# Performance work log

Hardware: AMD Instinct MI355X
Metric: run time of the kernel (lower is better)

Reference implementation:

```python
import jax, jax.numpy as jnp
import numpy as np

ITERN = 5  # hard-coded SqrtmLayer(cov_mat, 5)


def setup_inputs() -> dict:
    key = jax.random.key(0)
    k1, k2, k3 = jax.random.split(key, 3)
    B, C, H, W = 16, 64, 256, 256
    R = 8  # reduction
    x = jax.random.normal(k1, (B, C, H, W), dtype=jnp.float32)
    w1 = jax.random.normal(k2, (C // R, C), dtype=jnp.float32) * 0.1
    b1 = jnp.zeros((C // R,), dtype=jnp.float32)
    w2 = jax.random.normal(k3, (C, C // R), dtype=jnp.float32) * 0.1
    b2 = jnp.zeros((C,), dtype=jnp.float32)
    return {"x": x, "w1": w1, "b1": b1, "w2": w2, "b2": b2}


def _covpool(x):
    # x: [B, C, h, w].  y = x @ I_hat @ x^T with I_hat = (1/M)I - (1/M^2)J,
    # which equals centered covariance: (x_c @ x_c^T) / M.
    B, C, h, w = x.shape
    M = h * w
    xf = x.reshape(B, C, M)
    xc = xf - jnp.mean(xf, axis=-1, keepdims=True)
    return jnp.einsum('bcm,bdm->bcd', xc, xc) / M  # [B, C, C]


def _sqrtm_ns(cov, iterN):
    # Newton-Schulz iteration for matrix square root (per-batch [C,C]).
    B, C, _ = cov.shape
    I = jnp.eye(C, dtype=cov.dtype)
    I3 = 3.0 * I
    normA = jnp.einsum('bii->b', cov)  # trace
    A = cov / normA[:, None, None]
    ZY = 0.5 * (I3 - A)
    Y = jnp.matmul(A, ZY)
    Z = ZY
    for _ in range(1, iterN - 1):
        ZY = 0.5 * (I3 - jnp.matmul(Z, Y))
        Y = jnp.matmul(Y, ZY)
        Z = jnp.matmul(ZY, Z)
    ZY = 0.5 * jnp.matmul(Y, I3 - jnp.matmul(Z, Y))
    return ZY * jnp.sqrt(normA)[:, None, None]


def reference(x, w1, b1, w2, b2):
    # h,w < 1000 so the crop branch is identity (x_sub = x)
    cov = _covpool(x)                       # [B, C, C]
    cov_sqrt = _sqrtm_ns(cov, ITERN)        # [B, C, C]
    v = jnp.mean(cov_sqrt, axis=1)          # [B, C] (mean over rows, dim=1)
    hid = jax.nn.relu(jnp.einsum('bc,hc->bh', v, w1) + b1)
    att = jax.nn.sigmoid(jnp.einsum('bh,ch->bc', hid, w2) + b2)
    return att[:, :, None, None] * x
```

## Files before the change

kernel.cpp:

```cpp
#include <hip/hip_runtime.h>
#include <hip/hip_bf16.h>
#include <math.h>

#define BATCH 16
#define CH    64
#define MM    65536
#define PSTRIDE 4160
#define SF    68

typedef __attribute__((ext_vector_type(8))) short s16x8;
typedef __attribute__((ext_vector_type(4))) float f32x4;

__device__ __forceinline__ unsigned short f2bf(float f) {
    __hip_bfloat16 h = __float2bfloat16(f);
    return __builtin_bit_cast(unsigned short, h);
}
__device__ __forceinline__ float bf2f(unsigned short u) {
    return __builtin_bit_cast(float, (unsigned)u << 16);
}

__global__ __launch_bounds__(256, 3) void gram_mfma(const float* __restrict__ x,
                                                    float* __restrict__ part,
                                                    int nchunk, int chunk_m) {
    int blk = blockIdx.x;
    int b = blk / nchunk, chunk = blk - b * nchunk;
    int t = threadIdx.x, w = t >> 6, l = t & 63;
    int lr = l & 15, lg = l >> 4;
    int mwave = chunk_m >> 2;
    int nck = mwave >> 5;

    const float* xw = x + (size_t)b * CH * MM + (size_t)chunk * chunk_m +
                      (size_t)w * mwave + lg * 8;
    const float* rp0 = xw + (size_t)(lr)      * MM;
    const float* rp1 = xw + (size_t)(16 + lr) * MM;
    const float* rp2 = xw + (size_t)(32 + lr) * MM;
    const float* rp3 = xw + (size_t)(48 + lr) * MM;

    f32x4 acc[10];
    f32x4 accs[4];
    const f32x4 zero = {0.f, 0.f, 0.f, 0.f};
#pragma unroll
    for (int i = 0; i < 10; ++i) acc[i] = zero;
#pragma unroll
    for (int i = 0; i < 4; ++i) accs[i] = zero;

    s16x8 ones;
    {
        unsigned short* op1 = (unsigned short*)&ones;
#pragma unroll
        for (int i = 0; i < 8; ++i) op1[i] = 0x3F80;
    }

    float4 A0, A1, A2, A3, A4, A5, A6, A7;
    float4 B0, B1, B2, B3, B4, B5, B6, B7;

#define LOAD8(P, o) do {                                                      \
        P##0 = *(const float4*)(rp0 + (o));  P##1 = *(const float4*)(rp0 + (o) + 4); \
        P##2 = *(const float4*)(rp1 + (o));  P##3 = *(const float4*)(rp1 + (o) + 4); \
        P##4 = *(const float4*)(rp2 + (o));  P##5 = *(const float4*)(rp2 + (o) + 4); \
        P##6 = *(const float4*)(rp3 + (o));  P##7 = *(const float4*)(rp3 + (o) + 4); \
    } while (0)

#define CVT_ROW(va, vb, fr) do {                                              \
        unsigned short* fp = (unsigned short*)&(fr);                          \
        fp[0] = f2bf((va).x); fp[1] = f2bf((va).y);                           \
        fp[2] = f2bf((va).z); fp[3] = f2bf((va).w);                           \
        fp[4] = f2bf((vb).x); fp[5] = f2bf((vb).y);                           \
        fp[6] = f2bf((vb).z); fp[7] = f2bf((vb).w);                           \
    } while (0)

#define COMPUTE(P) do {                                                       \
        s16x8 fr0, fr1, fr2, fr3;                                             \
        CVT_ROW(P##0, P##1, fr0);                                             \
        CVT_ROW(P##2, P##3, fr1);                                             \
        CVT_ROW(P##4, P##5, fr2);                                             \
        CVT_ROW(P##6, P##7, fr3);                                             \
        acc[0] = __builtin_amdgcn_mfma_f32_16x16x32_bf16(fr0, fr0, acc[0], 0, 0, 0); \
        acc[1] = __builtin_amdgcn_mfma_f32_16x16x32_bf16(fr0, fr1, acc[1], 0, 0, 0); \
        acc[2] = __builtin_amdgcn_mfma_f32_16x16x32_bf16(fr0, fr2, acc[2], 0, 0, 0); \
        acc[3] = __builtin_amdgcn_mfma_f32_16x16x32_bf16(fr0, fr3, acc[3], 0, 0, 0); \
        acc[4] = __builtin_amdgcn_mfma_f32_16x16x32_bf16(fr1, fr1, acc[4], 0, 0, 0); \
        acc[5] = __builtin_amdgcn_mfma_f32_16x16x32_bf16(fr1, fr2, acc[5], 0, 0, 0); \
        acc[6] = __builtin_amdgcn_mfma_f32_16x16x32_bf16(fr1, fr3, acc[6], 0, 0, 0); \
        acc[7] = __builtin_amdgcn_mfma_f32_16x16x32_bf16(fr2, fr2, acc[7], 0, 0, 0); \
        acc[8] = __builtin_amdgcn_mfma_f32_16x16x32_bf16(fr2, fr3, acc[8], 0, 0, 0); \
        acc[9] = __builtin_amdgcn_mfma_f32_16x16x32_bf16(fr3, fr3, acc[9], 0, 0, 0); \
        accs[0] = __builtin_amdgcn_mfma_f32_16x16x32_bf16(ones, fr0, accs[0], 0, 0, 0); \
        accs[1] = __builtin_amdgcn_mfma_f32_16x16x32_bf16(ones, fr1, accs[1], 0, 0, 0); \
        accs[2] = __builtin_amdgcn_mfma_f32_16x16x32_bf16(ones, fr2, accs[2], 0, 0, 0); \
        accs[3] = __builtin_amdgcn_mfma_f32_16x16x32_bf16(ones, fr3, accs[3], 0, 0, 0); \
    } while (0)

    LOAD8(A, 0);
    for (int c = 0; c < nck; c += 2) {
        LOAD8(B, (c + 1) * 32);
        COMPUTE(A);
        if (c + 2 < nck) LOAD8(A, (c + 2) * 32);
        COMPUTE(B);
    }

#define UIDX(i, j) ((i) * 4 + (j) - ((i) * ((i) + 1)) / 2)

    __shared__ float xs[64 * 65];
    __shared__ float csum[64];
    for (int ww = 0; ww < 4; ++ww) {
        if (w == ww) {
#pragma unroll
            for (int i = 0; i < 4; ++i)
#pragma unroll
                for (int j = 0; j < 4; ++j)
                    if (i <= j) {
#pragma unroll
                        for (int jj = 0; jj < 4; ++jj) {
                            int r = i * 16 + lg * 4 + jj, cc = j * 16 + lr;
                            float v = acc[UIDX(i, j)][jj];
                            if (ww == 0) xs[r * 65 + cc] = v;
                            else         xs[r * 65 + cc] += v;
                        }
                    }
            if (l < 16) {
                if (ww == 0) {
                    csum[l]      = accs[0][0]; csum[16 + l] = accs[1][0];
                    csum[32 + l] = accs[2][0]; csum[48 + l] = accs[3][0];
                } else {
                    csum[l]      += accs[0][0]; csum[16 + l] += accs[1][0];
                    csum[32 + l] += accs[2][0]; csum[48 + l] += accs[3][0];
                }
            }
        }
        __syncthreads();
    }

    float* op = part + (size_t)blk * PSTRIDE;
#pragma unroll
    for (int rix = 0; rix < 16; ++rix) {
        int e = t + rix * 256;
        int r = e >> 6, cc = e & 63;
        float v = ((r >> 4) > (cc >> 4)) ? xs[cc * 65 + r] : xs[r * 65 + cc];
        __builtin_nontemporal_store(v, op + e);
    }
    if (t < 64) __builtin_nontemporal_store(csum[t], op + 4096 + t);
}

__global__ __launch_bounds__(256) void reduce_parts(const float* __restrict__ part,
                                                    float* __restrict__ red,
                                                    int nchunk) {
    int b = blockIdx.y;
    int i = blockIdx.x * 256 + threadIdx.x;
    if (i >= PSTRIDE / 4) return;
    const f32x4* p = reinterpret_cast<const f32x4*>(part + (size_t)b * nchunk * PSTRIDE) + i;
    f32x4 s = {0.f, 0.f, 0.f, 0.f};
    for (int ch = 0; ch < nchunk; ++ch) {
        f32x4 v = __builtin_nontemporal_load(p + (size_t)ch * (PSTRIDE / 4));
        s += v;
    }
    reinterpret_cast<f32x4*>(red + (size_t)b * PSTRIDE)[i] = s;
}

__device__ __forceinline__ void cvt_store(const float* __restrict__ M, int row,
                                          int col, unsigned short* Hp,
                                          unsigned short* Lp) {
    float4 v = *reinterpret_cast<const float4*>(M + row * SF + col);
    ushort4 h, lo;
    h.x = f2bf(v.x); lo.x = f2bf(v.x - bf2f(h.x));
    h.y = f2bf(v.y); lo.y = f2bf(v.y - bf2f(h.y));
    h.z = f2bf(v.z); lo.z = f2bf(v.z - bf2f(h.z));
    h.w = f2bf(v.w); lo.w = f2bf(v.w - bf2f(h.w));
    int byte = (row * 128 + col * 2) ^ ((row & 7) << 4);
    *reinterpret_cast<ushort4*>(reinterpret_cast<char*>(Hp) + byte) = h;
    *reinterpret_cast<ushort4*>(reinterpret_cast<char*>(Lp) + byte) = lo;
}

__device__ __forceinline__ void mm64(const float* __restrict__ A,
                                     const float* __restrict__ B,
                                     float* __restrict__ C,
                                     unsigned short* AHp, unsigned short* ALp,
                                     unsigned short* BHp, unsigned short* BLp,
                                     int t) {
    int w = t >> 6, l = t & 63, lg = l >> 4, lr = l & 15;
    __syncthreads();
#pragma unroll
    for (int r = 0; r < 4; ++r) {
        int e4 = t + r * 256;
        int row = e4 >> 4;
        int col = (e4 & 15) << 2;
        cvt_store(A, row, col, AHp, ALp);
        cvt_store(B, row, col, BHp, BLp);
    }
    __syncthreads();
    f32x4 acc[4];
    const f32x4 zero = {0.f, 0.f, 0.f, 0.f};
#pragma unroll
    for (int i = 0; i < 4; ++i) acc[i] = zero;
    int arow = w * 16 + lr;
#pragma unroll
    for (int kk = 0; kk < 2; ++kk) {
        int kbyte = kk * 64 + lg * 16;
        int abyte = (arow * 128 + kbyte) ^ ((arow & 7) << 4);
        s16x8 ah = *reinterpret_cast<const s16x8*>(reinterpret_cast<const char*>(AHp) + abyte);
        s16x8 al = *reinterpret_cast<const s16x8*>(reinterpret_cast<const char*>(ALp) + abyte);
#pragma unroll
        for (int ct = 0; ct < 4; ++ct) {
            int brow = ct * 16 + lr;
            int bbyte = (brow * 128 + kbyte) ^ ((brow & 7) << 4);
            s16x8 bh = *reinterpret_cast<const s16x8*>(reinterpret_cast<const char*>(BHp) + bbyte);
            s16x8 bl = *reinterpret_cast<const s16x8*>(reinterpret_cast<const char*>(BLp) + bbyte);
            acc[ct] = __builtin_amdgcn_mfma_f32_16x16x32_bf16(ah, bh, acc[ct], 0, 0, 0);
            acc[ct] = __builtin_amdgcn_mfma_f32_16x16x32_bf16(ah, bl, acc[ct], 0, 0, 0);
            acc[ct] = __builtin_amdgcn_mfma_f32_16x16x32_bf16(al, bh, acc[ct], 0, 0, 0);
        }
    }
#pragma unroll
    for (int ct = 0; ct < 4; ++ct)
#pragma unroll
        for (int j = 0; j < 4; ++j)
            C[(w * 16 + lg * 4 + j) * SF + ct * 16 + lr] = acc[ct][j];
    __syncthreads();
}

__global__ __launch_bounds__(256) void ns_att(const float* __restrict__ red,
                                              const float* __restrict__ w1,
                                              const float* __restrict__ b1,
                                              const float* __restrict__ w2,
                                              const float* __restrict__ b2,
                                              float* __restrict__ att) {
    __shared__ float BUF[5][64 * SF];
    __shared__ unsigned short AH[64 * 64], AL[64 * 64], BH[64 * 64], BL[64 * 64];
    __shared__ float sv[64];
    __shared__ float hid8[8];
    __shared__ float scal[2];

    int b = blockIdx.x, t = threadIdx.x;
    const float* pb = red + (size_t)b * PSTRIDE;

    if (t < 64) sv[t] = pb[4096 + t];
    __syncthreads();

    const float invM = 1.0f / (float)MM;
    const float invM2 = invM * invM;
#pragma unroll
    for (int r = 0; r < 4; ++r) {
        int e4 = t + r * 256;
        int row = e4 >> 4;
        int col = (e4 & 15) << 2;
        float4 g = *(reinterpret_cast<const float4*>(pb) + e4);
        float sr = sv[row] * invM2;
        BUF[0][row * SF + col]     = g.x * invM - sr * sv[col];
        BUF[0][row * SF + col + 1] = g.y * invM - sr * sv[col + 1];
        BUF[0][row * SF + col + 2] = g.z * invM - sr * sv[col + 2];
        BUF[0][row * SF + col + 3] = g.w * invM - sr * sv[col + 3];
    }
    __syncthreads();

    if (t == 0) {
        float tr = 0.f;
        for (int c = 0; c < 64; ++c) tr += BUF[0][c * SF + c];
        scal[0] = 1.0f / tr;
        scal[1] = sqrtf(tr);
    }
    __syncthreads();
    float itr = scal[0];
#pragma unroll
    for (int rr = 0; rr < 16; ++rr) {
        int e = t + rr * 256;
        BUF[0][(e >> 6) * SF + (e & 63)] *= itr;
    }

    float *pA = BUF[0], *pY = BUF[1], *pZ = BUF[2], *pT = BUF[3], *pS = BUF[4];

    mm64(pA, pA, pT, AH, AL, BH, BL, t);
#pragma unroll
    for (int rr = 0; rr < 16; ++rr) {
        int e = t + rr * 256;
        int r = e >> 6, c = e & 63;
        float a = pA[r * SF + c];
        pY[r * SF + c] = 1.5f * a - 0.5f * pT[r * SF + c];
        pZ[r * SF + c] = (r == c ? 1.5f : 0.f) - 0.5f * a;
    }

    for (int it = 0; it < 3; ++it) {
        mm64(pZ, pY, pT, AH, AL, BH, BL, t);
#pragma unroll
        for (int rr = 0; rr < 16; ++rr) {
            int e = t + rr * 256;
            int r = e >> 6, c = e & 63;
            pT[r * SF + c] = (r == c ? 1.5f : 0.f) - 0.5f * pT[r * SF + c];
        }
        mm64(pY, pT, pS, AH, AL, BH, BL, t);
        mm64(pT, pZ, pA, AH, AL, BH, BL, t);
        float* tmp;
        tmp = pY; pY = pS; pS = tmp;
        tmp = pZ; pZ = pA; pA = tmp;
    }
    mm64(pZ, pY, pT, AH, AL, BH, BL, t);
#pragma unroll
    for (int rr = 0; rr < 16; ++rr) {
        int e = t + rr * 256;
        int r = e >> 6, c = e & 63;
        pT[r * SF + c] = (r == c ? 1.5f : 0.f) - 0.5f * pT[r * SF + c];
    }
    mm64(pY, pT, pS, AH, AL, BH, BL, t);

    if (t < 64) {
        float v = 0.f;
        for (int i = 0; i < 64; ++i) v += pS[t * SF + i];
        sv[t] = v * scal[1] * (1.0f / 64.0f);
    }
    __syncthreads();
    if (t < 8) {
        float h = b1[t];
        for (int c = 0; c < 64; ++c) h += sv[c] * w1[t * 64 + c];
        hid8[t] = h > 0.f ? h : 0.f;
    }
    __syncthreads();
    if (t < 64) {
        float p = b2[t];
        for (int h = 0; h < 8; ++h) p += hid8[h] * w2[t * 8 + h];
        att[b * 64 + t] = 1.0f / (1.0f + expf(-p));
    }
}

__global__ __launch_bounds__(256) void scale_out(const float* __restrict__ x,
                                                 const float* __restrict__ att,
                                                 float* __restrict__ out) {
    size_t i = (size_t)blockIdx.x * blockDim.x + threadIdx.x;
    const size_t total4 = (size_t)BATCH * CH * MM / 4;
    const size_t stride = (size_t)gridDim.x * blockDim.x;
    const f32x4* x4 = reinterpret_cast<const f32x4*>(x);
    f32x4* o4 = reinterpret_cast<f32x4*>(out);
    for (; i < total4; i += stride) {
        int bc = (int)(i >> 14);
        float a = att[bc];
        f32x4 v = x4[i];
        v *= a;
        __builtin_nontemporal_store(v, o4 + i);
    }
}

extern "C" void kernel_launch(void* const* d_in, const int* in_sizes, int n_in,
                              void* d_out, int out_size, void* d_ws, size_t ws_size,
                              hipStream_t stream) {
    const float* x  = (const float*)d_in[0];
    const float* w1 = (const float*)d_in[1];
    const float* b1 = (const float*)d_in[2];
    const float* w2 = (const float*)d_in[3];
    const float* b2 = (const float*)d_in[4];
    float* out = (float*)d_out;
    float* ws  = (float*)d_ws;

    int nchunk = 64;
    for (;;) {
        size_t need = ((size_t)BATCH * nchunk * PSTRIDE + (size_t)BATCH * PSTRIDE +
                       (size_t)BATCH * CH) * sizeof(float);
        if (need <= ws_size || nchunk == 1) break;
        nchunk >>= 1;
    }
    int chunk_m = MM / nchunk;

    float* part = ws;
    float* red  = ws + (size_t)BATCH * nchunk * PSTRIDE;
    float* att  = red + (size_t)BATCH * PSTRIDE;

    gram_mfma<<<BATCH * nchunk, 256, 0, stream>>>(x, part, nchunk, chunk_m);
    reduce_parts<<<dim3((PSTRIDE / 4 + 255) / 256, BATCH), 256, 0, stream>>>(part, red, nchunk);
    ns_att<<<BATCH, 256, 0, stream>>>(red, w1, b1, w2, b2, att);
    scale_out<<<4096, 256, 0, stream>>>(x, att, out);
}
```

Before: 176.3 us.

## Restructure Newton-Schulz with fused epilogues, mat-vec tail, and reverse-order scale pass

The Newton-Schulz chain is reordered so the I3-0.5X update is fused into the matmul epilogue, and the first product is taken on Z rather than A. The last matmuls are replaced by a chain of matrix-vector products, since only the column mean of the result is needed. The trace now uses a wavefront shuffle reduction instead of a serial loop. The scale_out pass walks x in reverse order, likely to reuse data the gram kernel left in cache, but it now assumes total4 divides evenly by the grid stride.

```diff
diff --git a/kernel.cpp b/kernel.cpp
--- a/kernel.cpp
+++ b/kernel.cpp
@@ -171,6 +171,7 @@
     *reinterpret_cast<ushort4*>(reinterpret_cast<char*>(Lp) + byte) = lo;
 }
 
+template <int EPI>
 __device__ __forceinline__ void mm64(const float* __restrict__ A,
                                      const float* __restrict__ B,
                                      float* __restrict__ C,
@@ -213,8 +214,30 @@
 #pragma unroll
     for (int ct = 0; ct < 4; ++ct)
 #pragma unroll
-        for (int j = 0; j < 4; ++j)
-            C[(w * 16 + lg * 4 + j) * SF + ct * 16 + lr] = acc[ct][j];
+        for (int j = 0; j < 4; ++j) {
+            int r = w * 16 + lg * 4 + j, c = ct * 16 + lr;
+            float v = acc[ct][j];
+            if (EPI == 1) v = (r == c ? 1.5f : 0.f) - 0.5f * v;
+            C[r * SF + c] = v;
+        }
+    __syncthreads();
+}
+
+__device__ __forceinline__ void mv64(float* __restrict__ dst,
+                                     const float* __restrict__ M,
+                                     const float* __restrict__ src,
+                                     float* __restrict__ mvp, int t) {
+    int i = t & 63, q = t >> 6;
+    float p = 0.f;
+#pragma unroll
+    for (int jj = 0; jj < 16; ++jj) {
+        int j = q * 16 + jj;
+        float s = src ? src[j] : 1.f;
+        p = fmaf(M[j * SF + i], s, p);
+    }
+    mvp[q * 64 + i] = p;
+    __syncthreads();
+    if (t < 64) dst[t] = (mvp[t] + mvp[64 + t]) + (mvp[128 + t] + mvp[192 + t]);
     __syncthreads();
 }
 
@@ -226,7 +249,8 @@
                                               float* __restrict__ att) {
     __shared__ float BUF[5][64 * SF];
     __shared__ unsigned short AH[64 * 64], AL[64 * 64], BH[64 * 64], BL[64 * 64];
-    __shared__ float sv[64];
+    __shared__ float sv[64], u4s[64], vecA[64], vecB[64];
+    __shared__ float mvp[256];
     __shared__ float hid8[8];
     __shared__ float scal[2];
 
@@ -252,60 +276,41 @@
     }
     __syncthreads();
 
-    if (t == 0) {
-        float tr = 0.f;
-        for (int c = 0; c < 64; ++c) tr += BUF[0][c * SF + c];
-        scal[0] = 1.0f / tr;
-        scal[1] = sqrtf(tr);
+    if (t < 64) {
+        float d = BUF[0][t * SF + t];
+#pragma unroll
+        for (int m = 1; m < 64; m <<= 1) d += __shfl_xor(d, m);
+        if (t == 0) { scal[0] = 1.0f / d; scal[1] = sqrtf(d); }
     }
     __syncthreads();
     float itr = scal[0];
-#pragma unroll
-    for (int rr = 0; rr < 16; ++rr) {
-        int e = t + rr * 256;
-        BUF[0][(e >> 6) * SF + (e & 63)] *= itr;
-    }
-
-    float *pA = BUF[0], *pY = BUF[1], *pZ = BUF[2], *pT = BUF[3], *pS = BUF[4];
-
-    mm64(pA, pA, pT, AH, AL, BH, BL, t);
+
 #pragma unroll
     for (int rr = 0; rr < 16; ++rr) {
         int e = t + rr * 256;
         int r = e >> 6, c = e & 63;
-        float a = pA[r * SF + c];
-        pY[r * SF + c] = 1.5f * a - 0.5f * pT[r * SF + c];
-        pZ[r * SF + c] = (r == c ? 1.5f : 0.f) - 0.5f * a;
-    }
-
-    for (int it = 0; it < 3; ++it) {
-        mm64(pZ, pY, pT, AH, AL, BH, BL, t);
-#pragma unroll
-        for (int rr = 0; rr < 16; ++rr) {
-            int e = t + rr * 256;
-            int r = e >> 6, c = e & 63;
-            pT[r * SF + c] = (r == c ? 1.5f : 0.f) - 0.5f * pT[r * SF + c];
-        }
-        mm64(pY, pT, pS, AH, AL, BH, BL, t);
-        mm64(pT, pZ, pA, AH, AL, BH, BL, t);
-        float* tmp;
-        tmp = pY; pY = pS; pS = tmp;
-        tmp = pZ; pZ = pA; pA = tmp;
-    }
-    mm64(pZ, pY, pT, AH, AL, BH, BL, t);
-#pragma unroll
-    for (int rr = 0; rr < 16; ++rr) {
-        int e = t + rr * 256;
-        int r = e >> 6, c = e & 63;
-        pT[r * SF + c] = (r == c ? 1.5f : 0.f) - 0.5f * pT[r * SF + c];
-    }
-    mm64(pY, pT, pS, AH, AL, BH, BL, t);
-
-    if (t < 64) {
-        float v = 0.f;
-        for (int i = 0; i < 64; ++i) v += pS[t * SF + i];
-        sv[t] = v * scal[1] * (1.0f / 64.0f);
-    }
+        float a = BUF[0][r * SF + c] * itr;
+        BUF[0][r * SF + c] = a;
+        BUF[1][r * SF + c] = (r == c ? 1.5f : 0.f) - 0.5f * a;
+    }
+
+    mm64<0>(BUF[0], BUF[1], BUF[2], AH, AL, BH, BL, t);
+    mm64<1>(BUF[1], BUF[2], BUF[3], AH, AL, BH, BL, t);
+    mm64<0>(BUF[2], BUF[3], BUF[4], AH, AL, BH, BL, t);
+    mm64<0>(BUF[3], BUF[1], BUF[0], AH, AL, BH, BL, t);
+    mm64<1>(BUF[0], BUF[4], BUF[1], AH, AL, BH, BL, t);
+    mm64<0>(BUF[4], BUF[1], BUF[2], AH, AL, BH, BL, t);
+    mm64<0>(BUF[1], BUF[0], BUF[3], AH, AL, BH, BL, t);
+    mm64<1>(BUF[3], BUF[2], BUF[0], AH, AL, BH, BL, t);
+
+    mv64(vecA, BUF[2], nullptr, mvp, t);
+    mv64(u4s,  BUF[0], vecA,    mvp, t);
+    mv64(vecA, BUF[0], u4s,     mvp, t);
+    mv64(vecB, BUF[3], vecA,    mvp, t);
+    mv64(vecA, BUF[2], vecB,    mvp, t);
+    mv64(vecB, BUF[0], vecA,    mvp, t);
+
+    if (t < 64) sv[t] = (1.5f * u4s[t] - 0.5f * vecB[t]) * scal[1] * (1.0f / 64.0f);
     __syncthreads();
     if (t < 8) {
         float h = b1[t];
@@ -323,17 +328,20 @@
 __global__ __launch_bounds__(256) void scale_out(const float* __restrict__ x,
                                                  const float* __restrict__ att,
                                                  float* __restrict__ out) {
-    size_t i = (size_t)blockIdx.x * blockDim.x + threadIdx.x;
     const size_t total4 = (size_t)BATCH * CH * MM / 4;
     const size_t stride = (size_t)gridDim.x * blockDim.x;
     const f32x4* x4 = reinterpret_cast<const f32x4*>(x);
     f32x4* o4 = reinterpret_cast<f32x4*>(out);
-    for (; i < total4; i += stride) {
+    size_t base = (size_t)(gridDim.x - 1 - blockIdx.x) * blockDim.x + threadIdx.x;
+    int niter = (int)(total4 / stride);
+    size_t i = base + (size_t)(niter - 1) * stride;
+    for (int k = 0; k < niter; ++k) {
         int bc = (int)(i >> 14);
         float a = att[bc];
         f32x4 v = x4[i];
         v *= a;
         __builtin_nontemporal_store(v, o4 + i);
+        i -= stride;
     }
 }
 
```

After: 173.0 us. Within noise of the previous version (-1.9%).
